# Optimization experiments

Measured on AMD Instinct MI355X. Metric: run time of the kernel, lower is better.

## Reference

```python
import jax, jax.numpy as jnp
import numpy as np

NUM_EMBEDDINGS = 8192
EMBEDDING_DIM = 256
COMMITMENT_COST = 0.25


def setup_inputs() -> dict:
    key = jax.random.key(0)
    k1, k2 = jax.random.split(key)
    inputs = jax.random.normal(k1, (16, 2048, EMBEDDING_DIM), dtype=jnp.float32)
    # codebook initialized uniform(-1/K, 1/K) as in the torch module
    codebook = jax.random.uniform(
        k2, (NUM_EMBEDDINGS, EMBEDDING_DIM), dtype=jnp.float32,
        minval=-1.0 / NUM_EMBEDDINGS, maxval=1.0 / NUM_EMBEDDINGS)
    return {"inputs": inputs, "codebook": codebook}


def reference(inputs, codebook):
    B, T, D = inputs.shape
    flat = inputs.reshape(-1, D)                      # [BT, D]
    distances = (
        jnp.sum(flat * flat, axis=1, keepdims=True)
        + jnp.sum(codebook * codebook, axis=1)
        - 2.0 * jnp.matmul(flat, codebook.T)
    )
    idx = jnp.argmin(distances, axis=1)               # [BT]
    quantized = codebook[idx].reshape(B, T, D)        # gather == one-hot @ codebook
    e_latent_loss = jnp.mean((jax.lax.stop_gradient(quantized) - inputs) ** 2)
    q_latent_loss = jnp.mean((quantized - jax.lax.stop_gradient(inputs)) ** 2)
    loss = q_latent_loss + COMMITMENT_COST * e_latent_loss
    # straight-through estimator
    quantized_st = inputs + jax.lax.stop_gradient(quantized - inputs)
    return quantized_st, idx.reshape(B, T), loss
```

## Files before the change

### kernel.cpp

```cpp
#include <hip/hip_runtime.h>
#include <hip/hip_bf16.h>
#include <stdint.h>

#define D      256
#define K      8192
#define NROWS  32768
#define QELEMS 8388608

typedef __attribute__((ext_vector_type(8))) short bf16x8;
typedef __attribute__((ext_vector_type(4))) float f32x4;
typedef unsigned int u32;
typedef unsigned short u16;

__device__ __forceinline__ u16 f2bf(float f) {
    u32 b = __float_as_uint(f);
    return (u16)((b + 0x7fffu + ((b >> 16) & 1u)) >> 16);
}

__global__ __launch_bounds__(256) void vq_prep_kernel(
    const float* __restrict__ cb, u16* __restrict__ ch,
    float* __restrict__ se, float* __restrict__ loss_sum) {
    int row = blockIdx.x * 4 + (threadIdx.x >> 6);
    int l = threadIdx.x & 63;
    float4 v = *(const float4*)(cb + (size_t)row * D + l * 4);
    ushort4 o;
    o.x = f2bf(v.x); o.y = f2bf(v.y); o.z = f2bf(v.z); o.w = f2bf(v.w);
    *(ushort4*)(ch + (size_t)row * D + l * 4) = o;
    float s = v.x * v.x + v.y * v.y + v.z * v.z + v.w * v.w;
    #pragma unroll
    for (int off = 32; off > 0; off >>= 1) s += __shfl_down(s, off, 64);
    if (l == 0) se[row] = s;
    if (blockIdx.x == 0 && threadIdx.x == 0) *loss_sum = 0.f;
}

__global__ __launch_bounds__(256, 2) void vq_filter_kernel(
    const u16* __restrict__ ch, const float* __restrict__ x,
    const float* __restrict__ se, u32* __restrict__ cand)
{
    __shared__ float Mv[64 * 33];
    __shared__ u32   Mc[64 * 33];

    const int tid  = threadIdx.x;
    const int lane = tid & 63;
    const int wave = tid >> 6;
    const int l15  = lane & 15;
    const int l4   = lane >> 4;
    const int row0 = blockIdx.x * 64;

    bf16x8 Bf[4][8];
    #pragma unroll
    for (int nt = 0; nt < 4; ++nt) {
        const float* xr = x + (size_t)(row0 + nt * 16 + l15) * D + l4 * 8;
        #pragma unroll
        for (int c = 0; c < 8; ++c) {
            float4 a = *(const float4*)(xr + c * 32);
            float4 b = *(const float4*)(xr + c * 32 + 4);
            bf16x8 f;
            f[0] = (short)f2bf(a.x); f[1] = (short)f2bf(a.y);
            f[2] = (short)f2bf(a.z); f[3] = (short)f2bf(a.w);
            f[4] = (short)f2bf(b.x); f[5] = (short)f2bf(b.y);
            f[6] = (short)f2bf(b.z); f[7] = (short)f2bf(b.w);
            Bf[nt][c] = f;
        }
    }

    float b0[4], b1[4]; int c0[4], c1[4];
    #pragma unroll
    for (int nt = 0; nt < 4; ++nt) { b0[nt] = 1e30f; b1[nt] = 1e30f; c0[nt] = 0; c1[nt] = 0; }

    const u16* apl = ch + (size_t)(wave * 16 + l15) * D + l4 * 8;

#define LOAD_AF(AF, CT) do {                                                  \
    const u16* _p = apl + (size_t)(CT) * 16384;                               \
    _Pragma("unroll")                                                         \
    for (int c = 0; c < 8; ++c) (AF)[c] = *(const bf16x8*)(_p + c * 32);      \
} while (0)

#define COMP_TILE(AF, CT) do {                                                \
    const int k0 = (CT) << 6;                                                 \
    f32x4 sev = *(const f32x4*)(se + k0 + wave * 16 + l4 * 4);                \
    f32x4 acc[4];                                                             \
    _Pragma("unroll")                                                         \
    for (int nt = 0; nt < 4; ++nt) acc[nt] = (f32x4){0.f, 0.f, 0.f, 0.f};     \
    _Pragma("unroll")                                                         \
    for (int c = 0; c < 8; ++c) {                                             \
        acc[0] = __builtin_amdgcn_mfma_f32_16x16x32_bf16((AF)[c], Bf[0][c], acc[0], 0, 0, 0); \
        acc[1] = __builtin_amdgcn_mfma_f32_16x16x32_bf16((AF)[c], Bf[1][c], acc[1], 0, 0, 0); \
        acc[2] = __builtin_amdgcn_mfma_f32_16x16x32_bf16((AF)[c], Bf[2][c], acc[2], 0, 0, 0); \
        acc[3] = __builtin_amdgcn_mfma_f32_16x16x32_bf16((AF)[c], Bf[3][c], acc[3], 0, 0, 0); \
    }                                                                         \
    _Pragma("unroll")                                                         \
    for (int nt = 0; nt < 4; ++nt) {                                          \
        float t0 = fmaf(-2.f, acc[nt][0], sev[0]);                            \
        float t1 = fmaf(-2.f, acc[nt][1], sev[1]);                            \
        float t2 = fmaf(-2.f, acc[nt][2], sev[2]);                            \
        float t3 = fmaf(-2.f, acc[nt][3], sev[3]);                            \
        float tmn = fminf(fminf(t0, t1), fminf(t2, t3));                      \
        if (tmn < b1[nt]) {                                                   \
            _Pragma("unroll")                                                 \
            for (int r = 0; r < 4; ++r) {                                     \
                float t = fmaf(-2.f, acc[nt][r], sev[r]);                     \
                int  cv = k0 + wave * 16 + l4 * 4 + r;                        \
                bool in0 = t < b0[nt];                                        \
                bool in1 = t < b1[nt];                                        \
                float ob0 = b0[nt]; int oc0 = c0[nt];                         \
                b1[nt] = in0 ? ob0 : (in1 ? t  : b1[nt]);                     \
                c1[nt] = in0 ? oc0 : (in1 ? cv : c1[nt]);                     \
                b0[nt] = in0 ? t  : ob0;                                      \
                c0[nt] = in0 ? cv : oc0;                                      \
            }                                                                 \
        }                                                                     \
    }                                                                         \
} while (0)

    bf16x8 AfA[8], AfB[8];
    LOAD_AF(AfA, 0);
    #pragma unroll 1
    for (int ct = 0; ct < 128; ct += 2) {
        LOAD_AF(AfB, ct + 1);
        COMP_TILE(AfA, ct);
        if (ct + 2 < 128) LOAD_AF(AfA, ct + 2);
        COMP_TILE(AfB, ct + 1);
    }
#undef LOAD_AF
#undef COMP_TILE

    #pragma unroll
    for (int nt = 0; nt < 4; ++nt) {
        int rl = nt * 16 + l15;
        int g  = wave * 4 + l4;
        Mv[rl * 33 + g * 2]     = b0[nt];
        Mv[rl * 33 + g * 2 + 1] = b1[nt];
        Mc[rl * 33 + g * 2]     = (u32)c0[nt];
        Mc[rl * 33 + g * 2 + 1] = (u32)c1[nt];
    }
    __syncthreads();

    for (int tsk = tid; tsk < 512; tsk += 256) {
        int row = tsk >> 3, m = tsk & 7;
        const float* v  = Mv + row * 33 + m * 4;
        const u32*   cc = Mc + row * 33 + m * 4;
        float v00 = v[0],  v01 = v[1],  v10 = v[2],  v11 = v[3];
        u32   c00 = cc[0], c01 = cc[1], c10 = cc[2], c11 = cc[3];
        bool  aw  = v00 <= v10;
        u32   w0c = aw ? c00 : c10;
        float s1  = aw ? v10 : v00; u32 s1c = aw ? c10 : c00;
        float s2  = aw ? v01 : v11; u32 s2c = aw ? c01 : c11;
        u32   w1c = (s2 <= s1) ? s2c : s1c;
        cand[(size_t)(row0 + row) * 16 + m * 2]     = w0c;
        cand[(size_t)(row0 + row) * 16 + m * 2 + 1] = w1c;
    }
}

__global__ __launch_bounds__(1024) void vq_rescore_kernel(
    const float* __restrict__ x, const float* __restrict__ cb,
    const float* __restrict__ se, const u32* __restrict__ cand,
    float* __restrict__ out, float* __restrict__ loss_sum)
{
    const int wave = threadIdx.x >> 6;
    const int lane = threadIdx.x & 63;
    const int row  = blockIdx.x * 16 + wave;

    float4 xv = *(const float4*)(x + (size_t)row * D + lane * 4);
    float sx = xv.x * xv.x + xv.y * xv.y + xv.z * xv.z + xv.w * xv.w;
    #pragma unroll
    for (int o = 1; o < 64; o <<= 1) sx += __shfl_xor(sx, o, 64);

    u32 myc = cand[(size_t)row * 16 + (lane & 15)];
    float best = 1e30f; int bk = 0x7fffffff;
    #pragma unroll 4
    for (int j = 0; j < 16; ++j) {
        int code = __shfl((int)myc, j, 64);
        float4 ev = *(const float4*)(cb + (size_t)code * D + lane * 4);
        float p = xv.x * ev.x + xv.y * ev.y + xv.z * ev.z + xv.w * ev.w;
        #pragma unroll
        for (int o = 1; o < 64; o <<= 1) p += __shfl_xor(p, o, 64);
        float dist = (sx + se[code]) - 2.0f * p;
        if (dist < best || (dist == best && code < bk)) { best = dist; bk = code; }
    }

    float4 q = *(const float4*)(cb + (size_t)bk * D + lane * 4);
    *(float4*)(out + (size_t)row * D + lane * 4) = q;
    float dx = q.x - xv.x, dy = q.y - xv.y, dz = q.z - xv.z, dw = q.w - xv.w;
    float s = dx * dx + dy * dy + dz * dz + dw * dw;
    #pragma unroll
    for (int o = 1; o < 64; o <<= 1) s += __shfl_xor(s, o, 64);
    if (lane == 0) out[QELEMS + row] = (float)bk;

    __shared__ float red[16];
    if (lane == 0) red[wave] = s;
    __syncthreads();
    if (threadIdx.x == 0) {
        float t = 0.f;
        #pragma unroll
        for (int w2 = 0; w2 < 16; ++w2) t += red[w2];
        atomicAdd(loss_sum, t);
    }
}

__global__ void vq_fin_kernel(const float* __restrict__ loss_sum, float* __restrict__ out) {
    out[QELEMS + NROWS] = 1.25f * (*loss_sum) * (1.0f / (float)QELEMS);
}

extern "C" void kernel_launch(void* const* d_in, const int* in_sizes, int n_in,
                              void* d_out, int out_size, void* d_ws, size_t ws_size,
                              hipStream_t stream) {
    const float* x  = (const float*)d_in[0];
    const float* cb = (const float*)d_in[1];
    float* out = (float*)d_out;

    u16* ch = (u16*)d_out;

    char* ws = (char*)d_ws;
    float* loss_sum = (float*)ws;
    float* sebuf    = (float*)(ws + 4096);
    u32*   cand     = (u32*)(ws + 65536);

    vq_prep_kernel<<<K / 4, 256, 0, stream>>>(cb, ch, sebuf, loss_sum);
    vq_filter_kernel<<<NROWS / 64, 256, 0, stream>>>(ch, x, sebuf, cand);
    vq_rescore_kernel<<<NROWS / 16, 1024, 0, stream>>>(x, cb, sebuf, cand, out, loss_sum);
    vq_fin_kernel<<<1, 1, 0, stream>>>(loss_sum, out);
}
```

Baseline: 405.1 us.

## Stage codebook tiles through LDS with async global_load_lds triple buffering

The filter kernel now uses 512-thread blocks covering 128 rows. Codebook tiles are staged into shared memory with global_load_lds across a 3-deep buffer, so each tile is read once per block and shared between the two row halves. Before, every wave loaded its A-fragments straight from global memory. Codebook squared norms are now kept as bf16 in LDS, which cuts global traffic but introduces rounding error in the filter scores and a barrier per tile.

```diff
diff --git a/kernel.cpp b/kernel.cpp
--- a/kernel.cpp
+++ b/kernel.cpp
@@ -16,10 +16,13 @@
     u32 b = __float_as_uint(f);
     return (u16)((b + 0x7fffu + ((b >> 16) & 1u)) >> 16);
 }
+__device__ __forceinline__ float bf2f(u16 h) {
+    return __uint_as_float((u32)h << 16);
+}
 
 __global__ __launch_bounds__(256) void vq_prep_kernel(
     const float* __restrict__ cb, u16* __restrict__ ch,
-    float* __restrict__ se, float* __restrict__ loss_sum) {
+    float* __restrict__ se, u16* __restrict__ seh, float* __restrict__ loss_sum) {
     int row = blockIdx.x * 4 + (threadIdx.x >> 6);
     int l = threadIdx.x & 63;
     float4 v = *(const float4*)(cb + (size_t)row * D + l * 4);
@@ -29,28 +32,40 @@
     float s = v.x * v.x + v.y * v.y + v.z * v.z + v.w * v.w;
     #pragma unroll
     for (int off = 32; off > 0; off >>= 1) s += __shfl_down(s, off, 64);
-    if (l == 0) se[row] = s;
+    if (l == 0) { se[row] = s; seh[row] = f2bf(s); }
     if (blockIdx.x == 0 && threadIdx.x == 0) *loss_sum = 0.f;
 }
 
-__global__ __launch_bounds__(256, 2) void vq_filter_kernel(
+__global__ __launch_bounds__(512, 2) void vq_filter_kernel(
     const u16* __restrict__ ch, const float* __restrict__ x,
-    const float* __restrict__ se, u32* __restrict__ cand)
+    const u16* __restrict__ seh, u32* __restrict__ cand)
 {
-    __shared__ float Mv[64 * 33];
-    __shared__ u32   Mc[64 * 33];
+    __shared__ union {
+        u16 as[3][16384];
+        struct { float mv[128 * 33]; u32 mc[128 * 33]; } mg;
+    } S;
+    __shared__ u16 seL[8192];
 
     const int tid  = threadIdx.x;
     const int lane = tid & 63;
     const int wave = tid >> 6;
+    const int m_w  = wave & 3;
+    const int n_w  = wave >> 2;
     const int l15  = lane & 15;
     const int l4   = lane >> 4;
-    const int row0 = blockIdx.x * 64;
+    const int row0 = blockIdx.x * 128;
+
+    {
+        uint4* dl = (uint4*)seL;
+        const uint4* sg = (const uint4*)seh;
+        dl[tid] = sg[tid];
+        dl[tid + 512] = sg[tid + 512];
+    }
 
     bf16x8 Bf[4][8];
     #pragma unroll
     for (int nt = 0; nt < 4; ++nt) {
-        const float* xr = x + (size_t)(row0 + nt * 16 + l15) * D + l4 * 8;
+        const float* xr = x + (size_t)(row0 + n_w * 64 + nt * 16 + l15) * D + l4 * 8;
         #pragma unroll
         for (int c = 0; c < 8; ++c) {
             float4 a = *(const float4*)(xr + c * 32);
@@ -68,78 +83,92 @@
     #pragma unroll
     for (int nt = 0; nt < 4; ++nt) { b0[nt] = 1e30f; b1[nt] = 1e30f; c0[nt] = 0; c1[nt] = 0; }
 
-    const u16* apl = ch + (size_t)(wave * 16 + l15) * D + l4 * 8;
-
-#define LOAD_AF(AF, CT) do {                                                  \
-    const u16* _p = apl + (size_t)(CT) * 16384;                               \
+#define STAGE(TILE, BUF) do {                                                 \
+    const int _kn = (TILE) << 6;                                              \
     _Pragma("unroll")                                                         \
-    for (int c = 0; c < 8; ++c) (AF)[c] = *(const bf16x8*)(_p + c * 32);      \
+    for (int i = 0; i < 4; ++i) {                                             \
+        const u16* gp = ch + (size_t)(_kn + i * 16 + l15) * D + wave * 32 + l4 * 8; \
+        u16* lb = &S.as[(BUF)][(size_t)(wave * 4 + i) * 512];                 \
+        __builtin_amdgcn_global_load_lds(                                     \
+            (const __attribute__((address_space(1))) u32*)gp,                 \
+            (__attribute__((address_space(3))) u32*)lb, 16, 0, 0);            \
+    }                                                                         \
 } while (0)
 
-#define COMP_TILE(AF, CT) do {                                                \
-    const int k0 = (CT) << 6;                                                 \
-    f32x4 sev = *(const f32x4*)(se + k0 + wave * 16 + l4 * 4);                \
-    f32x4 acc[4];                                                             \
-    _Pragma("unroll")                                                         \
-    for (int nt = 0; nt < 4; ++nt) acc[nt] = (f32x4){0.f, 0.f, 0.f, 0.f};     \
-    _Pragma("unroll")                                                         \
-    for (int c = 0; c < 8; ++c) {                                             \
-        acc[0] = __builtin_amdgcn_mfma_f32_16x16x32_bf16((AF)[c], Bf[0][c], acc[0], 0, 0, 0); \
-        acc[1] = __builtin_amdgcn_mfma_f32_16x16x32_bf16((AF)[c], Bf[1][c], acc[1], 0, 0, 0); \
-        acc[2] = __builtin_amdgcn_mfma_f32_16x16x32_bf16((AF)[c], Bf[2][c], acc[2], 0, 0, 0); \
-        acc[3] = __builtin_amdgcn_mfma_f32_16x16x32_bf16((AF)[c], Bf[3][c], acc[3], 0, 0, 0); \
-    }                                                                         \
-    _Pragma("unroll")                                                         \
-    for (int nt = 0; nt < 4; ++nt) {                                          \
-        float t0 = fmaf(-2.f, acc[nt][0], sev[0]);                            \
-        float t1 = fmaf(-2.f, acc[nt][1], sev[1]);                            \
-        float t2 = fmaf(-2.f, acc[nt][2], sev[2]);                            \
-        float t3 = fmaf(-2.f, acc[nt][3], sev[3]);                            \
-        float tmn = fminf(fminf(t0, t1), fminf(t2, t3));                      \
-        if (tmn < b1[nt]) {                                                   \
-            _Pragma("unroll")                                                 \
-            for (int r = 0; r < 4; ++r) {                                     \
-                float t = fmaf(-2.f, acc[nt][r], sev[r]);                     \
-                int  cv = k0 + wave * 16 + l4 * 4 + r;                        \
-                bool in0 = t < b0[nt];                                        \
-                bool in1 = t < b1[nt];                                        \
-                float ob0 = b0[nt]; int oc0 = c0[nt];                         \
-                b1[nt] = in0 ? ob0 : (in1 ? t  : b1[nt]);                     \
-                c1[nt] = in0 ? oc0 : (in1 ? cv : c1[nt]);                     \
-                b0[nt] = in0 ? t  : ob0;                                      \
-                c0[nt] = in0 ? cv : oc0;                                      \
-            }                                                                 \
+#define EPI(NT, A) do {                                                       \
+    float t0 = fmaf(-2.f, (A)[0], _se0);                                      \
+    float t1 = fmaf(-2.f, (A)[1], _se1);                                      \
+    float t2 = fmaf(-2.f, (A)[2], _se2);                                      \
+    float t3 = fmaf(-2.f, (A)[3], _se3);                                      \
+    float tmn = fminf(fminf(t0, t1), fminf(t2, t3));                          \
+    if (tmn < b1[NT]) {                                                       \
+        float tv[4] = {t0, t1, t2, t3};                                       \
+        _Pragma("unroll")                                                     \
+        for (int r = 0; r < 4; ++r) {                                         \
+            float t = tv[r];                                                  \
+            int cv = _kt + m_w * 16 + l4 * 4 + r;                             \
+            bool in0 = t < b0[NT];                                            \
+            bool in1 = t < b1[NT];                                            \
+            float ob0 = b0[NT]; int oc0 = c0[NT];                             \
+            b1[NT] = in0 ? ob0 : (in1 ? t  : b1[NT]);                         \
+            c1[NT] = in0 ? oc0 : (in1 ? cv : c1[NT]);                         \
+            b0[NT] = in0 ? t  : ob0;                                          \
+            c0[NT] = in0 ? cv : oc0;                                          \
         }                                                                     \
     }                                                                         \
 } while (0)
 
-    bf16x8 AfA[8], AfB[8];
-    LOAD_AF(AfA, 0);
+#define BODY(T, DO_STAGE, VMN) do {                                           \
+    if (DO_STAGE) STAGE((T) + 2, ((T) + 2) % 3);                              \
+    asm volatile("s_waitcnt vmcnt(" #VMN ")" ::: "memory");                   \
+    __builtin_amdgcn_s_barrier();                                             \
+    const int _kt = (T) << 6;                                                 \
+    const u16* _as = &S.as[(T) % 3][0];                                       \
+    f32x4 acc0 = {0.f,0.f,0.f,0.f}, acc1 = {0.f,0.f,0.f,0.f};                 \
+    f32x4 acc2 = {0.f,0.f,0.f,0.f}, acc3 = {0.f,0.f,0.f,0.f};                 \
+    _Pragma("unroll")                                                         \
+    for (int c = 0; c < 8; ++c) {                                             \
+        bf16x8 Af = *(const bf16x8*)(_as + (size_t)(c * 4 + m_w) * 512 + lane * 8); \
+        acc0 = __builtin_amdgcn_mfma_f32_16x16x32_bf16(Af, Bf[0][c], acc0, 0, 0, 0); \
+        acc1 = __builtin_amdgcn_mfma_f32_16x16x32_bf16(Af, Bf[1][c], acc1, 0, 0, 0); \
+        acc2 = __builtin_amdgcn_mfma_f32_16x16x32_bf16(Af, Bf[2][c], acc2, 0, 0, 0); \
+        acc3 = __builtin_amdgcn_mfma_f32_16x16x32_bf16(Af, Bf[3][c], acc3, 0, 0, 0); \
+    }                                                                         \
+    ushort4 _sh = *(const ushort4*)(seL + _kt + m_w * 16 + l4 * 4);           \
+    float _se0 = bf2f(_sh.x), _se1 = bf2f(_sh.y);                             \
+    float _se2 = bf2f(_sh.z), _se3 = bf2f(_sh.w);                             \
+    EPI(0, acc0); EPI(1, acc1); EPI(2, acc2); EPI(3, acc3);                   \
+    __builtin_amdgcn_s_barrier();                                             \
+} while (0)
+
+    STAGE(0, 0);
+    STAGE(1, 1);
+    __syncthreads();
+
     #pragma unroll 1
-    for (int ct = 0; ct < 128; ct += 2) {
-        LOAD_AF(AfB, ct + 1);
-        COMP_TILE(AfA, ct);
-        if (ct + 2 < 128) LOAD_AF(AfA, ct + 2);
-        COMP_TILE(AfB, ct + 1);
-    }
-#undef LOAD_AF
-#undef COMP_TILE
+    for (int t = 0; t < 126; ++t) BODY(t, 1, 8);
+    BODY(126, 0, 4);
+    BODY(127, 0, 0);
+
+#undef BODY
+#undef EPI
+#undef STAGE
 
     #pragma unroll
     for (int nt = 0; nt < 4; ++nt) {
-        int rl = nt * 16 + l15;
-        int g  = wave * 4 + l4;
-        Mv[rl * 33 + g * 2]     = b0[nt];
-        Mv[rl * 33 + g * 2 + 1] = b1[nt];
-        Mc[rl * 33 + g * 2]     = (u32)c0[nt];
-        Mc[rl * 33 + g * 2 + 1] = (u32)c1[nt];
+        int rl = n_w * 64 + nt * 16 + l15;
+        int g  = m_w * 4 + l4;
+        S.mg.mv[rl * 33 + g * 2]     = b0[nt];
+        S.mg.mv[rl * 33 + g * 2 + 1] = b1[nt];
+        S.mg.mc[rl * 33 + g * 2]     = (u32)c0[nt];
+        S.mg.mc[rl * 33 + g * 2 + 1] = (u32)c1[nt];
     }
     __syncthreads();
 
-    for (int tsk = tid; tsk < 512; tsk += 256) {
+    for (int tsk = tid; tsk < 1024; tsk += 512) {
         int row = tsk >> 3, m = tsk & 7;
-        const float* v  = Mv + row * 33 + m * 4;
-        const u32*   cc = Mc + row * 33 + m * 4;
+        const float* v  = S.mg.mv + row * 33 + m * 4;
+        const u32*   cc = S.mg.mc + row * 33 + m * 4;
         float v00 = v[0],  v01 = v[1],  v10 = v[2],  v11 = v[3];
         u32   c00 = cc[0], c01 = cc[1], c10 = cc[2], c11 = cc[3];
         bool  aw  = v00 <= v10;
@@ -214,10 +243,11 @@
     char* ws = (char*)d_ws;
     float* loss_sum = (float*)ws;
     float* sebuf    = (float*)(ws + 4096);
+    u16*   seh      = (u16*)(ws + 40960);
     u32*   cand     = (u32*)(ws + 65536);
 
-    vq_prep_kernel<<<K / 4, 256, 0, stream>>>(cb, ch, sebuf, loss_sum);
-    vq_filter_kernel<<<NROWS / 64, 256, 0, stream>>>(ch, x, sebuf, cand);
+    vq_prep_kernel<<<K / 4, 256, 0, stream>>>(cb, ch, sebuf, seh, loss_sum);
+    vq_filter_kernel<<<NROWS / 128, 512, 0, stream>>>(ch, x, seh, cand);
     vq_rescore_kernel<<<NROWS / 16, 1024, 0, stream>>>(x, cb, sebuf, cand, out, loss_sum);
     vq_fin_kernel<<<1, 1, 0, stream>>>(loss_sum, out);
 }
```

After: 407.4 us. No clear change (+0.6%).
